# Optimization experiments

Hardware: AMD Instinct MI355X
Metric: run time of the kernel (lower is better)

## Reference

```python
import jax, jax.numpy as jnp
import numpy as np

DIM = 1024
NUM_HEADS = 16
HEAD_DIM = DIM // NUM_HEADS
SCALE = 1.0 / DIM ** 0.5  # NOTE: source scales by 1/sqrt(dim), not 1/sqrt(head_dim)


def setup_inputs() -> dict:
    key = jax.random.key(0)
    k1, k2, k3 = jax.random.split(key, 3)
    b, n = 4, 2048
    x = jax.random.normal(k1, (b, n, DIM), dtype=jnp.float32)
    w_qkv = jax.random.normal(k2, (DIM, 3 * DIM), dtype=jnp.float32) * (DIM ** -0.5)
    w_proj = jax.random.normal(k3, (DIM, DIM), dtype=jnp.float32) * (DIM ** -0.5)
    b_proj = jnp.zeros((DIM,), dtype=jnp.float32)
    return {"x": x, "w_qkv": w_qkv, "w_proj": w_proj, "b_proj": b_proj}


def reference(x, w_qkv, w_proj, b_proj):
    b, n, c = x.shape
    h, d = NUM_HEADS, HEAD_DIM
    qkv = (x @ w_qkv).reshape(b, n, 3, h, d)
    qkv = jnp.transpose(qkv, (2, 0, 3, 1, 4))  # [3, b, h, n, d]
    q, k, v = qkv[0], qkv[1], qkv[2]
    attn = jnp.einsum('bhqd,bhkd->bhqk', q, k) * SCALE
    attn = jax.nn.softmax(attn, axis=-1)
    out = jnp.einsum('bhqk,bhkd->bhqd', attn, v)  # [b, h, n, d]
    out = jnp.transpose(out, (0, 2, 1, 3)).reshape(b, n, c)
    return out @ w_proj + b_proj
```

## Files before the change

kernel.cpp:

```cpp
#include <hip/hip_runtime.h>
#include <cstdint>

typedef float f32x4 __attribute__((ext_vector_type(4)));
typedef __bf16 bf16x8 __attribute__((ext_vector_type(8)));
typedef unsigned short u16x8 __attribute__((ext_vector_type(8)));

__device__ __forceinline__ unsigned short f2bf(float f) {
  union { float f; unsigned u; } x; x.f = f;
  unsigned r = x.u + 0x7FFFu + ((x.u >> 16) & 1u);
  return (unsigned short)(r >> 16);
}

__device__ __forceinline__ void load_lds16(const void* g, void* l) {
  auto gp = reinterpret_cast<const __attribute__((address_space(1))) void*>(
      reinterpret_cast<uintptr_t>(g));
  auto lp = reinterpret_cast<__attribute__((address_space(3))) void*>(
      (unsigned)(reinterpret_cast<uintptr_t>(l)));
  __builtin_amdgcn_global_load_lds(gp, lp, 16, 0, 0);
}


__global__ __launch_bounds__(256) void cvt_x_kernel(const float* __restrict__ in,
                                                    unsigned short* __restrict__ out) {
  const int i = (blockIdx.x * 256 + threadIdx.x) * 8;
  const float4 a = *(const float4*)(in + i);
  const float4 b = *(const float4*)(in + i + 4);
  u16x8 o;
  o[0] = f2bf(a.x); o[1] = f2bf(a.y); o[2] = f2bf(a.z); o[3] = f2bf(a.w);
  o[4] = f2bf(b.x); o[5] = f2bf(b.y); o[6] = f2bf(b.z); o[7] = f2bf(b.w);
  *(u16x8*)(out + i) = o;
}

__global__ __launch_bounds__(256) void cvt_w_t_kernel(const float* __restrict__ W,
                                                      unsigned short* __restrict__ WT,
                                                      int Nw) {
  const int k = blockIdx.y * 256 + threadIdx.x;
  const int n0 = blockIdx.x * 8;
  const float* p = W + (size_t)k * Nw + n0;
  const float4 a = *(const float4*)p;
  const float4 b = *(const float4*)(p + 4);
  float v[8] = {a.x, a.y, a.z, a.w, b.x, b.y, b.z, b.w};
#pragma unroll
  for (int j = 0; j < 8; ++j)
    WT[(size_t)(n0 + j) * 1024 + k] = f2bf(v[j]);
}

__global__ __launch_bounds__(256) void vt_kernel(const unsigned short* __restrict__ V,
                                                 unsigned short* __restrict__ VT) {
  const int n = blockIdx.x * 256 + threadIdx.x;
  const int d0 = blockIdx.y * 8;
  const int bh = blockIdx.z;
  const u16x8 v = *(const u16x8*)(V + (size_t)(bh * 2048 + n) * 64 + d0);
#pragma unroll
  for (int j = 0; j < 8; ++j)
    VT[((size_t)bh * 64 + d0 + j) * 2048 + n] = v[j];
}


template <int EPI>
__global__ __launch_bounds__(256) void gemm_bt(const unsigned short* __restrict__ A,
                                               const unsigned short* __restrict__ BT,
                                               unsigned short* __restrict__ oQ,
                                               unsigned short* __restrict__ oK,
                                               unsigned short* __restrict__ oV,
                                               float* __restrict__ oF,
                                               const float* __restrict__ bias,
                                               int Ncols) {
  constexpr int K = 1024;
  __shared__ unsigned short As[128 * 64];
  __shared__ unsigned short Bs[128 * 64];
  const int tid = threadIdx.x, lane = tid & 63, w = tid >> 6;
  const int wr = w >> 1, wc = w & 1;

  const int nwgx = gridDim.x;
  int id = blockIdx.y * nwgx + blockIdx.x;
  const int cpx = (nwgx * gridDim.y) >> 3;
  id = (id & 7) * cpx + (id >> 3);
  const int mBase = (id / nwgx) * 128, nBase = (id % nwgx) * 128;

  f32x4 acc[4][4];
#pragma unroll
  for (int m = 0; m < 4; ++m)
#pragma unroll
    for (int n = 0; n < 4; ++n)
#pragma unroll
      for (int r = 0; r < 4; ++r) acc[m][n][r] = 0.0f;

  const int srow = lane >> 3;
  const int scol = (lane & 7) * 8;
  const int l15 = lane & 15, g8 = (lane >> 4) * 8;

  for (int k0 = 0; k0 < K; k0 += 64) {
    __syncthreads();
#pragma unroll
    for (int i = 0; i < 4; ++i) {
      const int c = i * 4 + w;
      load_lds16(A + (size_t)(mBase + c * 8 + srow) * K + k0 + scol, &As[c * 512]);
      load_lds16(BT + (size_t)(nBase + c * 8 + srow) * K + k0 + scol, &Bs[c * 512]);
    }
    __syncthreads();
    bf16x8 af[4][2], bfr[4][2];
#pragma unroll
    for (int x = 0; x < 4; ++x)
#pragma unroll
      for (int kc = 0; kc < 2; ++kc) {
        af[x][kc] = *(const bf16x8*)&As[(wr * 64 + x * 16 + l15) * 64 + kc * 32 + g8];
        bfr[x][kc] = *(const bf16x8*)&Bs[(wc * 64 + x * 16 + l15) * 64 + kc * 32 + g8];
      }
#pragma unroll
    for (int m = 0; m < 4; ++m)
#pragma unroll
      for (int n = 0; n < 4; ++n)
#pragma unroll
        for (int kc = 0; kc < 2; ++kc)
          acc[m][n] = __builtin_amdgcn_mfma_f32_16x16x32_bf16(af[m][kc], bfr[n][kc],
                                                              acc[m][n], 0, 0, 0);
  }

  const int r0 = (lane >> 4) * 4, c0 = lane & 15;
  if (EPI == 0) {
#pragma unroll
    for (int n = 0; n < 4; ++n) {
      const int col = nBase + wc * 64 + n * 16 + c0;
      const int t = col >> 10, rem = col & 1023;
      const int h = rem >> 6, d = rem & 63;
      unsigned short* dst = (t == 0) ? oQ : ((t == 1) ? oK : oV);
      const float sc = (t == 0) ? 0.03125f * 1.44269504088896f : 1.0f;
#pragma unroll
      for (int m = 0; m < 4; ++m) {
        const int row = mBase + wr * 64 + m * 16 + r0;
        const int b = row >> 11, nn = row & 2047;
        const size_t base = ((size_t)((b * 16 + h) * 2048 + nn)) * 64 + d;
#pragma unroll
        for (int r = 0; r < 4; ++r)
          dst[base + (size_t)r * 64] = f2bf(acc[m][n][r] * sc);
      }
    }
  } else {
#pragma unroll
    for (int n = 0; n < 4; ++n) {
      const int col = nBase + wc * 64 + n * 16 + c0;
      const float bv = bias[col];
#pragma unroll
      for (int m = 0; m < 4; ++m) {
        const int row = mBase + wr * 64 + m * 16 + r0;
#pragma unroll
        for (int r = 0; r < 4; ++r)
          oF[(size_t)(row + r) * Ncols + col] = acc[m][n][r] + bv;
      }
    }
  }
}


__global__ __launch_bounds__(256) void attn_kernel(const unsigned short* __restrict__ Q,
                                                   const unsigned short* __restrict__ Kt,
                                                   const unsigned short* __restrict__ VT,
                                                   unsigned short* __restrict__ O) {
  __shared__ unsigned short Ks[64 * 64];
  __shared__ unsigned short Vs[64 * 64];
  __shared__ unsigned short Ps[4][32 * 64];
  const int tid = threadIdx.x, lane = tid & 63, w = tid >> 6;

  int id = blockIdx.y * gridDim.x + blockIdx.x;
  id = (id & 7) * 128 + (id >> 3);
  const int bh = id >> 4, qt = id & 15;

  const int b = bh >> 4, h = bh & 15;
  const int l15 = lane & 15, g = lane >> 4;
  const unsigned short* Qp = Q + ((size_t)bh * 2048 + qt * 128 + w * 32) * 64;
  const unsigned short* Kp = Kt + (size_t)bh * 2048 * 64;
  const unsigned short* Vp = VT + (size_t)bh * 64 * 2048;

  bf16x8 qf[2][2];
#pragma unroll
  for (int m = 0; m < 2; ++m)
#pragma unroll
    for (int kc = 0; kc < 2; ++kc)
      qf[m][kc] = *(const bf16x8*)(Qp + (m * 16 + l15) * 64 + kc * 32 + g * 8);

  float lsum[2][4];
  f32x4 accO[2][4];
#pragma unroll
  for (int m = 0; m < 2; ++m)
#pragma unroll
    for (int r = 0; r < 4; ++r) {
      lsum[m][r] = 0.0f;
#pragma unroll
      for (int dk = 0; dk < 4; ++dk) accO[m][dk][r] = 0.0f;
    }

  const int srow = lane >> 3;
  const int scb = ((lane & 7) * 16) ^ (srow << 4);

  for (int kt = 0; kt < 32; ++kt) {
    const int k0 = kt * 64;
    __syncthreads();
#pragma unroll
    for (int i = 0; i < 2; ++i) {
      const int c = i * 4 + w;
      const int row = c * 8 + srow;
      load_lds16(Kp + (size_t)(k0 + row) * 64 + (scb >> 1), &Ks[c * 512]);
      load_lds16(Vp + (size_t)row * 2048 + k0 + (scb >> 1), &Vs[c * 512]);
    }
    __syncthreads();

    bf16x8 kfr[4][2];
#pragma unroll
    for (int kf = 0; kf < 4; ++kf) {
      const int row = kf * 16 + l15;
#pragma unroll
      for (int kc = 0; kc < 2; ++kc) {
        const int cb = (kc * 64 + g * 16) ^ ((row & 7) << 4);
        kfr[kf][kc] = *(const bf16x8*)((const char*)Ks + row * 128 + cb);
      }
    }

#pragma unroll
    for (int m = 0; m < 2; ++m) {
      f32x4 s[4];
#pragma unroll
      for (int kf = 0; kf < 4; ++kf) {
#pragma unroll
        for (int r = 0; r < 4; ++r) s[kf][r] = 0.0f;
#pragma unroll
        for (int kc = 0; kc < 2; ++kc)
          s[kf] = __builtin_amdgcn_mfma_f32_16x16x32_bf16(qf[m][kc], kfr[kf][kc],
                                                          s[kf], 0, 0, 0);
      }
#pragma unroll
      for (int kf = 0; kf < 4; ++kf)
#pragma unroll
        for (int r = 0; r < 4; ++r) {
          const float p = __builtin_amdgcn_exp2f(s[kf][r]);
          lsum[m][r] += p;
          const int rowp = m * 16 + g * 4 + r;
          const int cb = ((kf * 16 + l15) * 2) ^ ((rowp & 7) << 4);
          *(__bf16*)((char*)Ps[w] + rowp * 128 + cb) = (__bf16)p;
        }
    }

    bf16x8 vfr[4][2];
#pragma unroll
    for (int dk = 0; dk < 4; ++dk) {
      const int row = dk * 16 + l15;
#pragma unroll
      for (int kc = 0; kc < 2; ++kc) {
        const int cb = (kc * 64 + g * 16) ^ ((row & 7) << 4);
        vfr[dk][kc] = *(const bf16x8*)((const char*)Vs + row * 128 + cb);
      }
    }
#pragma unroll
    for (int m = 0; m < 2; ++m) {
      bf16x8 pf[2];
      const int rowa = m * 16 + l15;
#pragma unroll
      for (int kc = 0; kc < 2; ++kc) {
        const int cb = (kc * 64 + g * 16) ^ ((rowa & 7) << 4);
        pf[kc] = *(const bf16x8*)((const char*)Ps[w] + rowa * 128 + cb);
      }
#pragma unroll
      for (int dk = 0; dk < 4; ++dk)
#pragma unroll
        for (int kc = 0; kc < 2; ++kc)
          accO[m][dk] = __builtin_amdgcn_mfma_f32_16x16x32_bf16(pf[kc], vfr[dk][kc],
                                                                accO[m][dk], 0, 0, 0);
    }
  }

#pragma unroll
  for (int m = 0; m < 2; ++m)
#pragma unroll
    for (int r = 0; r < 4; ++r) {
      float l = lsum[m][r];
      l += __shfl_xor(l, 1);
      l += __shfl_xor(l, 2);
      l += __shfl_xor(l, 4);
      l += __shfl_xor(l, 8);
      const float inv = 1.0f / l;
      const int nrow = qt * 128 + w * 32 + m * 16 + g * 4 + r;
      const size_t base = ((size_t)b * 2048 + nrow) * 1024 + h * 64 + l15;
#pragma unroll
      for (int dk = 0; dk < 4; ++dk)
        O[base + dk * 16] = f2bf(accO[m][dk][r] * inv);
    }
}


extern "C" void kernel_launch(void* const* d_in, const int* in_sizes, int n_in,
                              void* d_out, int out_size, void* d_ws, size_t ws_size,
                              hipStream_t stream) {
  const float* x = (const float*)d_in[0];
  const float* w_qkv = (const float*)d_in[1];
  const float* w_proj = (const float*)d_in[2];
  const float* b_proj = (const float*)d_in[3];

  char* ws = (char*)d_ws;
  unsigned short* xb     = (unsigned short*)(ws);
  unsigned short* wqkvT  = (unsigned short*)(ws + 16777216);
  unsigned short* wprojT = (unsigned short*)(ws + 23068672);
  unsigned short* Qb     = (unsigned short*)(ws + 25165824);
  unsigned short* Kb     = (unsigned short*)(ws + 41943040);
  unsigned short* Vb     = (unsigned short*)(ws + 58720256);
  unsigned short* VTb    = (unsigned short*)(ws + 75497472);
  unsigned short* AOb    = (unsigned short*)(ws + 92274688);

  cvt_x_kernel<<<4096, 256, 0, stream>>>(x, xb);
  cvt_w_t_kernel<<<dim3(384, 4), 256, 0, stream>>>(w_qkv, wqkvT, 3072);
  cvt_w_t_kernel<<<dim3(128, 4), 256, 0, stream>>>(w_proj, wprojT, 1024);
  gemm_bt<0><<<dim3(24, 64), 256, 0, stream>>>(xb, wqkvT, Qb, Kb, Vb, nullptr, nullptr, 3072);
  vt_kernel<<<dim3(8, 8, 64), 256, 0, stream>>>(Vb, VTb);
  attn_kernel<<<dim3(16, 64), 256, 0, stream>>>(Qb, Kb, VTb, AOb);
  gemm_bt<1><<<dim3(8, 64), 256, 0, stream>>>(AOb, wprojT, nullptr, nullptr, nullptr,
                                              (float*)d_out, b_proj, 1024);
}
```

Before: 343.1 us.

## Fuse V transpose into QKV GEMM and rework attention with 32x32 MFMA and double buffering

The QKV GEMM epilogue now writes V directly in transposed layout, which removes the separate vt_kernel launch and its extra global round trip. The attention kernel switches to 32x32x16 MFMAs and computes S transposed, so the exponentiated P tile is packed with v_cvt_pk_bf16_f32 and redistributed with v_permlane32_swap instead of going through LDS. K/V tiles are double-buffered so the next tile's async loads overlap compute, with one barrier per iteration. The changes add register pressure and rely on the MI355-specific permlane swap instruction, and correctness depends on the lane mapping being right. The softmax still has no max subtraction, same as before.

Result: faster. 302.6 us (-11.8%).

```diff
diff --git a/kernel.cpp b/kernel.cpp
--- a/kernel.cpp
+++ b/kernel.cpp
@@ -2,7 +2,9 @@
 #include <cstdint>
 
 typedef float f32x4 __attribute__((ext_vector_type(4)));
+typedef float f32x16 __attribute__((ext_vector_type(16)));
 typedef __bf16 bf16x8 __attribute__((ext_vector_type(8)));
+typedef unsigned short u16x4 __attribute__((ext_vector_type(4)));
 typedef unsigned short u16x8 __attribute__((ext_vector_type(8)));
 
 __device__ __forceinline__ unsigned short f2bf(float f) {
@@ -45,24 +47,13 @@
     WT[(size_t)(n0 + j) * 1024 + k] = f2bf(v[j]);
 }
 
-__global__ __launch_bounds__(256) void vt_kernel(const unsigned short* __restrict__ V,
-                                                 unsigned short* __restrict__ VT) {
-  const int n = blockIdx.x * 256 + threadIdx.x;
-  const int d0 = blockIdx.y * 8;
-  const int bh = blockIdx.z;
-  const u16x8 v = *(const u16x8*)(V + (size_t)(bh * 2048 + n) * 64 + d0);
-#pragma unroll
-  for (int j = 0; j < 8; ++j)
-    VT[((size_t)bh * 64 + d0 + j) * 2048 + n] = v[j];
-}
-
 
 template <int EPI>
 __global__ __launch_bounds__(256) void gemm_bt(const unsigned short* __restrict__ A,
                                                const unsigned short* __restrict__ BT,
                                                unsigned short* __restrict__ oQ,
                                                unsigned short* __restrict__ oK,
-                                               unsigned short* __restrict__ oV,
+                                               unsigned short* __restrict__ oVT,
                                                float* __restrict__ oF,
                                                const float* __restrict__ bias,
                                                int Ncols) {
@@ -124,16 +115,28 @@
       const int col = nBase + wc * 64 + n * 16 + c0;
       const int t = col >> 10, rem = col & 1023;
       const int h = rem >> 6, d = rem & 63;
-      unsigned short* dst = (t == 0) ? oQ : ((t == 1) ? oK : oV);
-      const float sc = (t == 0) ? 0.03125f * 1.44269504088896f : 1.0f;
-#pragma unroll
-      for (int m = 0; m < 4; ++m) {
-        const int row = mBase + wr * 64 + m * 16 + r0;
-        const int b = row >> 11, nn = row & 2047;
-        const size_t base = ((size_t)((b * 16 + h) * 2048 + nn)) * 64 + d;
-#pragma unroll
-        for (int r = 0; r < 4; ++r)
-          dst[base + (size_t)r * 64] = f2bf(acc[m][n][r] * sc);
+      if (t == 2) {
+#pragma unroll
+        for (int m = 0; m < 4; ++m) {
+          const int row = mBase + wr * 64 + m * 16 + r0;
+          const int b = row >> 11, nn = row & 2047;
+          u16x4 o;
+#pragma unroll
+          for (int r = 0; r < 4; ++r) o[r] = f2bf(acc[m][n][r]);
+          *(u16x4*)(oVT + ((size_t)((b * 16 + h) * 64 + d)) * 2048 + nn) = o;
+        }
+      } else {
+        unsigned short* dst = (t == 0) ? oQ : oK;
+        const float sc = (t == 0) ? 0.03125f * 1.44269504088896f : 1.0f;
+#pragma unroll
+        for (int m = 0; m < 4; ++m) {
+          const int row = mBase + wr * 64 + m * 16 + r0;
+          const int b = row >> 11, nn = row & 2047;
+          const size_t base = ((size_t)((b * 16 + h) * 2048 + nn)) * 64 + d;
+#pragma unroll
+          for (int r = 0; r < 4; ++r)
+            dst[base + (size_t)r * 64] = f2bf(acc[m][n][r] * sc);
+        }
       }
     }
   } else {
@@ -157,133 +160,131 @@
                                                    const unsigned short* __restrict__ Kt,
                                                    const unsigned short* __restrict__ VT,
                                                    unsigned short* __restrict__ O) {
-  __shared__ unsigned short Ks[64 * 64];
-  __shared__ unsigned short Vs[64 * 64];
-  __shared__ unsigned short Ps[4][32 * 64];
+  __shared__ unsigned short Ks[2][64 * 64];
+  __shared__ unsigned short Vs[2][64 * 64];
+  __shared__ float Ls[4][32];
   const int tid = threadIdx.x, lane = tid & 63, w = tid >> 6;
 
   int id = blockIdx.y * gridDim.x + blockIdx.x;
   id = (id & 7) * 128 + (id >> 3);
   const int bh = id >> 4, qt = id & 15;
-
   const int b = bh >> 4, h = bh & 15;
-  const int l15 = lane & 15, g = lane >> 4;
+  const int l31 = lane & 31, hi = lane >> 5;
+
   const unsigned short* Qp = Q + ((size_t)bh * 2048 + qt * 128 + w * 32) * 64;
   const unsigned short* Kp = Kt + (size_t)bh * 2048 * 64;
   const unsigned short* Vp = VT + (size_t)bh * 64 * 2048;
 
-  bf16x8 qf[2][2];
-#pragma unroll
-  for (int m = 0; m < 2; ++m)
-#pragma unroll
-    for (int kc = 0; kc < 2; ++kc)
-      qf[m][kc] = *(const bf16x8*)(Qp + (m * 16 + l15) * 64 + kc * 32 + g * 8);
-
-  float lsum[2][4];
-  f32x4 accO[2][4];
-#pragma unroll
-  for (int m = 0; m < 2; ++m)
-#pragma unroll
-    for (int r = 0; r < 4; ++r) {
-      lsum[m][r] = 0.0f;
-#pragma unroll
-      for (int dk = 0; dk < 4; ++dk) accO[m][dk][r] = 0.0f;
-    }
+  bf16x8 qf[4];
+#pragma unroll
+  for (int ss = 0; ss < 4; ++ss)
+    qf[ss] = *(const bf16x8*)(Qp + l31 * 64 + ss * 16 + hi * 8);
+
+  f32x16 accO[2];
+#pragma unroll
+  for (int db = 0; db < 2; ++db)
+#pragma unroll
+    for (int r = 0; r < 16; ++r) accO[db][r] = 0.0f;
+  float ls = 0.0f;
 
   const int srow = lane >> 3;
   const int scb = ((lane & 7) * 16) ^ (srow << 4);
 
-  for (int kt = 0; kt < 32; ++kt) {
-    const int k0 = kt * 64;
-    __syncthreads();
+  auto STAGE = [&](int bufi, int kt_) {
+    const int k0_ = kt_ * 64;
 #pragma unroll
     for (int i = 0; i < 2; ++i) {
       const int c = i * 4 + w;
       const int row = c * 8 + srow;
-      load_lds16(Kp + (size_t)(k0 + row) * 64 + (scb >> 1), &Ks[c * 512]);
-      load_lds16(Vp + (size_t)row * 2048 + k0 + (scb >> 1), &Vs[c * 512]);
+      load_lds16(Kp + (size_t)(k0_ + row) * 64 + (scb >> 1), &Ks[bufi][c * 512]);
+      load_lds16(Vp + (size_t)row * 2048 + k0_ + (scb >> 1), &Vs[bufi][c * 512]);
+    }
+  };
+
+  STAGE(0, 0);
+  __syncthreads();
+
+  for (int kt = 0; kt < 32; ++kt) {
+    const int cur = kt & 1;
+    if (kt + 1 < 32) STAGE(cur ^ 1, kt + 1);
+
+    const char* KsB = (const char*)Ks[cur];
+    const char* VsB = (const char*)Vs[cur];
+
+    f32x16 st[2];
+#pragma unroll
+    for (int kb = 0; kb < 2; ++kb) {
+      f32x16 s;
+#pragma unroll
+      for (int r = 0; r < 16; ++r) s[r] = 0.0f;
+      const int row = kb * 32 + l31;
+      const int sw = (row & 7) << 4;
+#pragma unroll
+      for (int ss = 0; ss < 4; ++ss) {
+        const bf16x8 kf = *(const bf16x8*)(KsB + row * 128 + ((ss * 32 + hi * 16) ^ sw));
+        s = __builtin_amdgcn_mfma_f32_32x32x16_bf16(kf, qf[ss], s, 0, 0, 0);
+      }
+      st[kb] = s;
+    }
+
+    unsigned pk[2][4][2];
+#pragma unroll
+    for (int kb = 0; kb < 2; ++kb) {
+#pragma unroll
+      for (int r = 0; r < 16; ++r) {
+        const float p = __builtin_amdgcn_exp2f(st[kb][r]);
+        st[kb][r] = p;
+        ls += p;
+      }
+#pragma unroll
+      for (int m2 = 0; m2 < 4; ++m2)
+#pragma unroll
+        for (int c = 0; c < 2; ++c)
+          asm("v_cvt_pk_bf16_f32 %0, %1, %2"
+              : "=v"(pk[kb][m2][c])
+              : "v"(st[kb][m2 * 4 + 2 * c]), "v"(st[kb][m2 * 4 + 2 * c + 1]));
+    }
+
+    bf16x8 pa[4];
+#pragma unroll
+    for (int s2 = 0; s2 < 4; ++s2) {
+      const int kb = s2 >> 1, t = s2 & 1;
+      union { unsigned u[4]; bf16x8 v; } fr;
+#pragma unroll
+      for (int c = 0; c < 2; ++c) {
+        unsigned x = pk[kb][2 * t][c];
+        unsigned y = pk[kb][2 * t + 1][c];
+        asm("v_permlane32_swap_b32 %0, %1" : "+v"(x), "+v"(y));
+        fr.u[c] = x;
+        fr.u[2 + c] = y;
+      }
+      pa[s2] = fr.v;
+    }
+
+#pragma unroll
+    for (int db = 0; db < 2; ++db) {
+      const int row = db * 32 + l31;
+      const int sw = (row & 7) << 4;
+#pragma unroll
+      for (int s2 = 0; s2 < 4; ++s2) {
+        const bf16x8 vf = *(const bf16x8*)(VsB + row * 128 + ((s2 * 32 + hi * 16) ^ sw));
+        accO[db] = __builtin_amdgcn_mfma_f32_32x32x16_bf16(pa[s2], vf, accO[db], 0, 0, 0);
+      }
     }
     __syncthreads();
-
-    bf16x8 kfr[4][2];
-#pragma unroll
-    for (int kf = 0; kf < 4; ++kf) {
-      const int row = kf * 16 + l15;
-#pragma unroll
-      for (int kc = 0; kc < 2; ++kc) {
-        const int cb = (kc * 64 + g * 16) ^ ((row & 7) << 4);
-        kfr[kf][kc] = *(const bf16x8*)((const char*)Ks + row * 128 + cb);
-      }
-    }
-
-#pragma unroll
-    for (int m = 0; m < 2; ++m) {
-      f32x4 s[4];
-#pragma unroll
-      for (int kf = 0; kf < 4; ++kf) {
-#pragma unroll
-        for (int r = 0; r < 4; ++r) s[kf][r] = 0.0f;
-#pragma unroll
-        for (int kc = 0; kc < 2; ++kc)
-          s[kf] = __builtin_amdgcn_mfma_f32_16x16x32_bf16(qf[m][kc], kfr[kf][kc],
-                                                          s[kf], 0, 0, 0);
-      }
-#pragma unroll
-      for (int kf = 0; kf < 4; ++kf)
-#pragma unroll
-        for (int r = 0; r < 4; ++r) {
-          const float p = __builtin_amdgcn_exp2f(s[kf][r]);
-          lsum[m][r] += p;
-          const int rowp = m * 16 + g * 4 + r;
-          const int cb = ((kf * 16 + l15) * 2) ^ ((rowp & 7) << 4);
-          *(__bf16*)((char*)Ps[w] + rowp * 128 + cb) = (__bf16)p;
-        }
-    }
-
-    bf16x8 vfr[4][2];
-#pragma unroll
-    for (int dk = 0; dk < 4; ++dk) {
-      const int row = dk * 16 + l15;
-#pragma unroll
-      for (int kc = 0; kc < 2; ++kc) {
-        const int cb = (kc * 64 + g * 16) ^ ((row & 7) << 4);
-        vfr[dk][kc] = *(const bf16x8*)((const char*)Vs + row * 128 + cb);
-      }
-    }
-#pragma unroll
-    for (int m = 0; m < 2; ++m) {
-      bf16x8 pf[2];
-      const int rowa = m * 16 + l15;
-#pragma unroll
-      for (int kc = 0; kc < 2; ++kc) {
-        const int cb = (kc * 64 + g * 16) ^ ((rowa & 7) << 4);
-        pf[kc] = *(const bf16x8*)((const char*)Ps[w] + rowa * 128 + cb);
-      }
-#pragma unroll
-      for (int dk = 0; dk < 4; ++dk)
-#pragma unroll
-        for (int kc = 0; kc < 2; ++kc)
-          accO[m][dk] = __builtin_amdgcn_mfma_f32_16x16x32_bf16(pf[kc], vfr[dk][kc],
-                                                                accO[m][dk], 0, 0, 0);
-    }
   }
 
-#pragma unroll
-  for (int m = 0; m < 2; ++m)
-#pragma unroll
-    for (int r = 0; r < 4; ++r) {
-      float l = lsum[m][r];
-      l += __shfl_xor(l, 1);
-      l += __shfl_xor(l, 2);
-      l += __shfl_xor(l, 4);
-      l += __shfl_xor(l, 8);
-      const float inv = 1.0f / l;
-      const int nrow = qt * 128 + w * 32 + m * 16 + g * 4 + r;
-      const size_t base = ((size_t)b * 2048 + nrow) * 1024 + h * 64 + l15;
-#pragma unroll
-      for (int dk = 0; dk < 4; ++dk)
-        O[base + dk * 16] = f2bf(accO[m][dk][r] * inv);
-    }
+  ls += __shfl_xor(ls, 32);
+  if (hi == 0) Ls[w][l31] = 1.0f / ls;
+
+#pragma unroll
+  for (int r = 0; r < 16; ++r) {
+    const int ql = (r & 3) + 8 * (r >> 2) + 4 * hi;
+    const float inv = Ls[w][ql];
+    const size_t base = ((size_t)b * 2048 + qt * 128 + w * 32 + ql) * 1024 + h * 64 + l31;
+    O[base] = f2bf(accO[0][r] * inv);
+    O[base + 32] = f2bf(accO[1][r] * inv);
+  }
 }
 
 
@@ -301,15 +302,13 @@
   unsigned short* wprojT = (unsigned short*)(ws + 23068672);
   unsigned short* Qb     = (unsigned short*)(ws + 25165824);
   unsigned short* Kb     = (unsigned short*)(ws + 41943040);
-  unsigned short* Vb     = (unsigned short*)(ws + 58720256);
-  unsigned short* VTb    = (unsigned short*)(ws + 75497472);
-  unsigned short* AOb    = (unsigned short*)(ws + 92274688);
+  unsigned short* VTb    = (unsigned short*)(ws + 58720256);
+  unsigned short* AOb    = (unsigned short*)(ws + 75497472);
 
   cvt_x_kernel<<<4096, 256, 0, stream>>>(x, xb);
   cvt_w_t_kernel<<<dim3(384, 4), 256, 0, stream>>>(w_qkv, wqkvT, 3072);
   cvt_w_t_kernel<<<dim3(128, 4), 256, 0, stream>>>(w_proj, wprojT, 1024);
-  gemm_bt<0><<<dim3(24, 64), 256, 0, stream>>>(xb, wqkvT, Qb, Kb, Vb, nullptr, nullptr, 3072);
-  vt_kernel<<<dim3(8, 8, 64), 256, 0, stream>>>(Vb, VTb);
+  gemm_bt<0><<<dim3(24, 64), 256, 0, stream>>>(xb, wqkvT, Qb, Kb, VTb, nullptr, nullptr, 3072);
   attn_kernel<<<dim3(16, 64), 256, 0, stream>>>(Qb, Kb, VTb, AOb);
   gemm_bt<1><<<dim3(8, 64), 256, 0, stream>>>(AOb, wprojT, nullptr, nullptr, nullptr,
                                               (float*)d_out, b_proj, 1024);
```
